# Optimization experiments

Hardware: AMD Instinct MI355X
Metric: run time of the kernel (lower is better)

Reference implementation:

```python
import jax, jax.numpy as jnp
import numpy as np
import math

N_HEADS = 4
N_ITERS = 2  # SSFormer n=2; each loop iteration recomputes the same values (no feedback in the original code)
BN_EPS = 1e-5


def _attention(q, k, v):
    """SSTransformer: multi-head cross-attention over flattened spatial dims.
    q,k,v: [B, C, H, W] -> returns [B, C, L] with L = H*W.
    """
    b, c = q.shape[0], q.shape[1]
    L = q.shape[2] * q.shape[3]
    ch = c // N_HEADS
    scale = 1.0 / math.sqrt(math.sqrt(ch))
    qf = (q.reshape(b * N_HEADS, ch, L) * scale)
    kf = (k.reshape(b * N_HEADS, ch, L) * scale)
    vf = v.reshape(b * N_HEADS, ch, L)
    # weight: [B*H, t, s]
    w = jnp.einsum('bct,bcs->bts', qf, kf)
    w = jax.nn.softmax(w.astype(jnp.float32), axis=-1).astype(w.dtype)
    a = jnp.einsum('bts,bcs->bct', w, vf)
    return a.reshape(b, c, L)


def setup_inputs() -> dict:
    key = jax.random.key(0)
    k1, k2, k3, k4 = jax.random.split(key, 4)
    B, C, H, W = 8, 512, 32, 32
    c = jax.random.normal(k1, (B, C, H, W), dtype=jnp.float32)
    e = jax.random.normal(k2, (B, C, H, W), dtype=jnp.float32)
    conv_w = jax.random.normal(k3, (C, C, 1, 1), dtype=jnp.float32) / math.sqrt(C)
    conv_b = jax.random.normal(k4, (C,), dtype=jnp.float32) * 0.02
    bn_gamma = jnp.ones((C,), dtype=jnp.float32)
    bn_beta = jnp.zeros((C,), dtype=jnp.float32)
    return {"c": c, "e": e, "conv_w": conv_w, "conv_b": conv_b,
            "bn_gamma": bn_gamma, "bn_beta": bn_beta}


def reference(c, e, conv_w, conv_b, bn_gamma, bn_beta):
    bs, ch, h, w = c.shape
    L = h * w
    for _ in range(N_ITERS):
        _c = _attention(e, c, c)                       # [B, C, L]
        _e = _attention(_c.reshape(bs, ch, h, w), e, e)  # [B, C, L]
    _e = _e.reshape(bs, ch, h, w)
    # Proj: 1x1 conv + BatchNorm2d (training-mode batch stats) + Swish
    x = jnp.einsum('oc,bchw->bohw', conv_w.reshape(ch, ch), _e) + conv_b[None, :, None, None]
    mean = jnp.mean(x, axis=(0, 2, 3), keepdims=True)
    var = jnp.var(x, axis=(0, 2, 3), keepdims=True)
    xn = (x - mean) * jax.lax.rsqrt(var + BN_EPS)
    xn = xn * bn_gamma[None, :, None, None] + bn_beta[None, :, None, None]
    return xn * jax.nn.sigmoid(xn)
```

## Files before the change

### kernel.cpp

```cpp
#include <hip/hip_runtime.h>
#include <hip/hip_bf16.h>

typedef __attribute__((ext_vector_type(8))) short short8;
typedef __attribute__((ext_vector_type(4))) float floatx4;
typedef __attribute__((ext_vector_type(4))) float f32x4;
typedef unsigned short u16;
typedef unsigned int u32;
typedef __attribute__((ext_vector_type(2))) unsigned int u32x2;
typedef __attribute__((ext_vector_type(4))) unsigned int u32x4;
typedef __attribute__((ext_vector_type(8))) unsigned short ushort8;

#define LSEQ 1024
#define CHD  128
#define CEXP 0.12751744900425577f
#define THR_RAW 62.73318f

static __device__ __forceinline__ u16 f2b(float f) {
  __hip_bfloat16 h = __float2bfloat16(f);
  return *reinterpret_cast<u16*>(&h);
}
static __device__ __forceinline__ u32 cvtpk(float a, float b) {
  u32 r;
  asm("v_cvt_pk_bf16_f32 %0, %1, %2" : "=v"(r) : "v"(a), "v"(b));
  return r;
}
static __device__ __forceinline__ float exp2f_fast(float x) {
  float r;
  asm("v_exp_f32 %0, %1" : "=v"(r) : "v"(x));
  return r;
}
static __device__ __forceinline__ void gl_lds16(const void* g, void* l) {
  __builtin_amdgcn_global_load_lds((__attribute__((address_space(1))) const void*)g,
                                   (__attribute__((address_space(3))) void*)l, 16, 0, 0);
}

__global__ __launch_bounds__(256) void k_prep(const float* __restrict__ cin,
                                              const float* __restrict__ ein,
                                              u16* __restrict__ cV, u16* __restrict__ cT,
                                              u16* __restrict__ eV, u16* __restrict__ eT) {
  __shared__ u16 tile[32][72];
  int z = blockIdx.z;
  const float* in = (z < 32) ? cin : ein;
  u16* outV = (z < 32) ? cV : eV;
  u16* outT = (z < 32) ? cT : eT;
  int bh = z & 31, c0 = blockIdx.y * 32, s0 = blockIdx.x * 64;
  int tid = threadIdx.x;
  int cl = tid >> 3, sc = tid & 7;
  size_t off = ((size_t)bh * CHD + c0 + cl) * LSEQ + s0 + sc * 8;
  f32x4 a = *(const f32x4*)(in + off);
  f32x4 b = *(const f32x4*)(in + off + 4);
  u32x4 u;
  u[0] = cvtpk(a[0], a[1]); u[1] = cvtpk(a[2], a[3]);
  u[2] = cvtpk(b[0], b[1]); u[3] = cvtpk(b[2], b[3]);
  *(u32x4*)(outV + off) = u;
  *(u32x4*)&tile[cl][sc * 8] = u;
  __syncthreads();
  int sl = tid >> 2, cc = tid & 3;
  ushort8 v;
#pragma unroll
  for (int j = 0; j < 8; ++j) v[j] = tile[cc * 8 + j][sl];
  *(ushort8*)(outT + ((size_t)bh * LSEQ + s0 + sl) * CHD + c0 + cc * 8) = v;
}

__global__ __launch_bounds__(256) void k_wcvt(const float* __restrict__ w, u16* __restrict__ wb,
                                              float* __restrict__ zbuf ) {
  int tid = threadIdx.x;
  int base = (blockIdx.x * 256 + tid) * 8;
  f32x4 a = *(const f32x4*)(w + base);
  f32x4 b = *(const f32x4*)(w + base + 4);
  u32x4 u;
  u[0] = cvtpk(a[0], a[1]); u[1] = cvtpk(a[2], a[3]);
  u[2] = cvtpk(b[0], b[1]); u[3] = cvtpk(b[2], b[3]);
  *(u32x4*)(wb + base) = u;
  if (blockIdx.x == 0) {
    f32x4 z; z[0]=0.f; z[1]=0.f; z[2]=0.f; z[3]=0.f;
    *(f32x4*)(zbuf + tid * 4) = z;
  }
}

__global__ __launch_bounds__(256) void k_attn(const u16* __restrict__ eT,
                                              const u16* __restrict__ cT,
                                              const u16* __restrict__ cV,
                                              const u16* __restrict__ eV,
                                              u16* __restrict__ outT) {
  __shared__ char ldsbuf[73728];

  int bh = blockIdx.x, tt = blockIdx.y;
  int tid = threadIdx.x;
  int w = tid >> 6, lane = tid & 63;
  int lo = lane & 15, hi = lane >> 4;
  int t0 = tt * 64 + w * 16;

  char* pw = ldsbuf + 65536 + w * 2048 + lo * 128;
  int sw = (lo & 7) << 4;

  auto stageK = [&](int buf, int sb, const char* kTb) {
    char* dst = ldsbuf + buf * 16384;
#pragma unroll
    for (int it = 0; it < 4; ++it) {
      int bb = it * 4096 + tid * 16;
      int row = bb >> 8;
      int cb = (bb & 255) ^ ((row & 7) << 4);
      gl_lds16(kTb + (size_t)(sb * 64 + row) * 256 + cb, dst + bb);
    }
  };
  auto stageV = [&](int buf, int sb, const char* vb) {
    char* dst = ldsbuf + 32768 + buf * 16384;
#pragma unroll
    for (int it = 0; it < 4; ++it) {
      int bb = it * 4096 + tid * 16;
      int row = bb >> 7;
      int cb = (bb & 127) ^ ((row & 7) << 4);
      gl_lds16(vb + (size_t)row * 2048 + sb * 128 + cb, dst + bb);
    }
  };

  short8 bq[4];
  floatx4 oacc[8];
  float m_r, l_r;

  auto flash = [&](const char* kTb, const char* vb) {
    m_r = -1e30f; l_r = 0.f;
#pragma unroll
    for (int i = 0; i < 8; ++i) { oacc[i][0]=0.f; oacc[i][1]=0.f; oacc[i][2]=0.f; oacc[i][3]=0.f; }
    stageK(0, 0, kTb); stageV(0, 0, vb);
    __syncthreads();
    int cur = 0;
    for (int sb = 0; sb < 16; ++sb) {
      if (sb < 15) { stageK(cur ^ 1, sb + 1, kTb); stageV(cur ^ 1, sb + 1, vb); }
      const char* ldsK = ldsbuf + cur * 16384;
      const char* ldsV = ldsbuf + 32768 + cur * 16384;

      float sa[4][4];
      __builtin_amdgcn_s_setprio(1);
#pragma unroll
      for (int ss = 0; ss < 4; ++ss) {
        floatx4 acc; acc[0]=0.f; acc[1]=0.f; acc[2]=0.f; acc[3]=0.f;
        int row = ss * 16 + lo;
#pragma unroll
        for (int ks = 0; ks < 4; ++ks) {
          int cbyte = (ks * 64 + hi * 16) ^ ((row & 7) << 4);
          short8 a = *(const short8*)(ldsK + row * 256 + cbyte);
          acc = __builtin_amdgcn_mfma_f32_16x16x32_bf16(a, bq[ks], acc, 0, 0, 0);
        }
#pragma unroll
        for (int r = 0; r < 4; ++r) sa[ss][r] = acc[r];
      }
      __builtin_amdgcn_s_setprio(0);

      float x0 = fmaxf(fmaxf(sa[0][0], sa[0][1]), sa[0][2]);
      float x1 = fmaxf(fmaxf(sa[0][3], sa[1][0]), sa[1][1]);
      float x2 = fmaxf(fmaxf(sa[1][2], sa[1][3]), sa[2][0]);
      float x3 = fmaxf(fmaxf(sa[2][1], sa[2][2]), sa[2][3]);
      float x4 = fmaxf(fmaxf(sa[3][0], sa[3][1]), sa[3][2]);
      float bm = fmaxf(fmaxf(fmaxf(x0, x1), fmaxf(x2, x3)), fmaxf(x4, sa[3][3]));
      bm = fmaxf(bm, __shfl_xor(bm, 16));
      bm = fmaxf(bm, __shfl_xor(bm, 32));

      bool stay = __all(bm - m_r <= THR_RAW);
      if (!stay) {
        float mn = fmaxf(m_r, bm);
        float corr = exp2f_fast((m_r - mn) * CEXP);
        m_r = mn;
        l_r *= corr;
#pragma unroll
        for (int i = 0; i < 8; ++i) {
          oacc[i][0] *= corr; oacc[i][1] *= corr; oacc[i][2] *= corr; oacc[i][3] *= corr;
        }
      }
      float mnC = m_r * CEXP;

      float rs = 0.f;
#pragma unroll
      for (int ss = 0; ss < 4; ++ss)
#pragma unroll
        for (int r = 0; r < 4; ++r) {
          float p = exp2f_fast(__builtin_fmaf(sa[ss][r], CEXP, -mnC));
          sa[ss][r] = p;
          rs += p;
        }
      rs += __shfl_xor(rs, 16);
      rs += __shfl_xor(rs, 32);
      l_r += rs;

#pragma unroll
      for (int ss = 0; ss < 4; ++ss) {
        u32x2 pk;
        pk[0] = cvtpk(sa[ss][0], sa[ss][1]);
        pk[1] = cvtpk(sa[ss][2], sa[ss][3]);
        *(u32x2*)(pw + ((ss * 32 + hi * 8) ^ sw)) = pk;
      }
      asm volatile("" ::: "memory");

      short8 bp0 = *(const short8*)(pw + ((hi * 16) ^ sw));
      short8 bp1 = *(const short8*)(pw + ((64 + hi * 16) ^ sw));
      __builtin_amdgcn_s_setprio(1);
#pragma unroll
      for (int mt = 0; mt < 8; ++mt) {
        int crow = mt * 16 + lo;
        const char* va = ldsV + crow * 128;
        int vsw = (crow & 7) << 4;
        short8 a0 = *(const short8*)(va + ((hi * 16) ^ vsw));
        short8 a1 = *(const short8*)(va + ((64 + hi * 16) ^ vsw));
        oacc[mt] = __builtin_amdgcn_mfma_f32_16x16x32_bf16(a0, bp0, oacc[mt], 0, 0, 0);
        oacc[mt] = __builtin_amdgcn_mfma_f32_16x16x32_bf16(a1, bp1, oacc[mt], 0, 0, 0);
      }
      __builtin_amdgcn_s_setprio(0);
      __syncthreads();
      cur ^= 1;
    }
  };

  const u16* qbase = eT + ((size_t)bh * LSEQ + t0 + lo) * CHD + hi * 8;
#pragma unroll
  for (int ks = 0; ks < 4; ++ks) bq[ks] = *(const short8*)(qbase + ks * 32);

  flash((const char*)(cT + (size_t)bh * LSEQ * CHD),
        (const char*)(cV + (size_t)bh * CHD * LSEQ));

  {
    float inv = 1.0f / l_r;
    char* ot = ldsbuf + w * 4096;
#pragma unroll
    for (int mt = 0; mt < 8; ++mt) {
      u32x2 pk;
      pk[0] = cvtpk(oacc[mt][0] * inv, oacc[mt][1] * inv);
      pk[1] = cvtpk(oacc[mt][2] * inv, oacc[mt][3] * inv);
      *(u32x2*)(ot + lo * 256 + ((mt * 32 + hi * 8) ^ ((lo & 7) << 4))) = pk;
    }
    asm volatile("" ::: "memory");
#pragma unroll
    for (int ks = 0; ks < 4; ++ks) {
      int cb = (ks * 64 + hi * 16) ^ ((lo & 7) << 4);
      bq[ks] = *(const short8*)(ot + lo * 256 + cb);
    }
  }
  __syncthreads();

  flash((const char*)(eT + (size_t)bh * LSEQ * CHD),
        (const char*)(eV + (size_t)bh * CHD * LSEQ));

  float inv = 1.0f / l_r;
  char* ot = ldsbuf + w * 4096;
#pragma unroll
  for (int mt = 0; mt < 8; ++mt) {
    u32x2 pk;
    pk[0] = cvtpk(oacc[mt][0] * inv, oacc[mt][1] * inv);
    pk[1] = cvtpk(oacc[mt][2] * inv, oacc[mt][3] * inv);
    *(u32x2*)(ot + lo * 256 + ((mt * 32 + hi * 8) ^ ((lo & 7) << 4))) = pk;
  }
  asm volatile("" ::: "memory");
  u16* orow = outT + ((size_t)bh * LSEQ + t0 + lo) * CHD;
#pragma unroll
  for (int it = 0; it < 4; ++it) {
    int cb = (it * 64 + hi * 16) ^ ((lo & 7) << 4);
    ushort8 d = *(const ushort8*)(ot + lo * 256 + cb);
    *(ushort8*)(orow + it * 32 + hi * 8) = d;
  }
}

__global__ __launch_bounds__(256) void k_proj(const u16* __restrict__ Wm,
                                              const u16* __restrict__ eT,
                                              const float* __restrict__ bias,
                                              u16* __restrict__ x,
                                              float* __restrict__ chsum,
                                              float* __restrict__ chsq) {
  __shared__ char lds[65536];
  int lt = blockIdx.x, ot = blockIdx.y;
  int b = lt >> 3;
  int l0b = (lt & 7) * 128;
  int o0 = ot * 128;
  int tid = threadIdx.x, w = tid >> 6, lane = tid & 63, lo = lane & 15, hi = lane >> 4;
  int wm = w >> 1, wn = w & 1;
  const char* Wb = (const char*)Wm;
  const char* eTb = (const char*)eT;

  auto stageA = [&](int buf, int kb) {
    char* dst = lds + buf * 16384;
#pragma unroll
    for (int it = 0; it < 4; ++it) {
      int bb = it * 4096 + tid * 16;
      int row = bb >> 7;
      int cb = (bb & 127) ^ ((row & 7) << 4);
      gl_lds16(Wb + (size_t)(o0 + row) * 1024 + kb * 128 + cb, dst + bb);
    }
  };
  auto stageB = [&](int buf, int kb) {
    char* dst = lds + 32768 + buf * 16384;
    int page = b * 4 + (kb >> 1);
    int choff = (kb & 1) * 128;
#pragma unroll
    for (int it = 0; it < 4; ++it) {
      int bb = it * 4096 + tid * 16;
      int row = bb >> 7;
      int cb = (bb & 127) ^ ((row & 7) << 4);
      gl_lds16(eTb + ((size_t)page * 1024 + l0b + row) * 256 + choff + cb, dst + bb);
    }
  };

  floatx4 acc[4][4];
#pragma unroll
  for (int i = 0; i < 4; ++i)
#pragma unroll
    for (int j = 0; j < 4; ++j) { acc[i][j][0]=0.f; acc[i][j][1]=0.f; acc[i][j][2]=0.f; acc[i][j][3]=0.f; }

  stageA(0, 0); stageB(0, 0);
  __syncthreads();
  int cur = 0;

  for (int kb = 0; kb < 8; ++kb) {
    if (kb < 7) { stageA(cur ^ 1, kb + 1); stageB(cur ^ 1, kb + 1); }
    const char* A = lds + cur * 16384;
    const char* B = lds + 32768 + cur * 16384;
#pragma unroll
    for (int kk = 0; kk < 2; ++kk) {
      short8 af[4], bf[4];
#pragma unroll
      for (int mi = 0; mi < 4; ++mi) {
        int row = wm * 64 + mi * 16 + lo;
        af[mi] = *(const short8*)(A + row * 128 + ((kk * 64 + hi * 16) ^ ((row & 7) << 4)));
      }
#pragma unroll
      for (int ni = 0; ni < 4; ++ni) {
        int row = wn * 64 + ni * 16 + lo;
        bf[ni] = *(const short8*)(B + row * 128 + ((kk * 64 + hi * 16) ^ ((row & 7) << 4)));
      }
      __builtin_amdgcn_s_setprio(1);
#pragma unroll
      for (int mi = 0; mi < 4; ++mi)
#pragma unroll
        for (int ni = 0; ni < 4; ++ni)
          acc[mi][ni] = __builtin_amdgcn_mfma_f32_16x16x32_bf16(af[mi], bf[ni], acc[mi][ni], 0, 0, 0);
      __builtin_amdgcn_s_setprio(0);
    }
    __syncthreads();
    cur ^= 1;
  }

#pragma unroll
  for (int mi = 0; mi < 4; ++mi) {
#pragma unroll
    for (int r = 0; r < 4; ++r) {
      int o = o0 + wm * 64 + mi * 16 + hi * 4 + r;
      float bv = bias[o];
      float s = 0.f, q = 0.f;
#pragma unroll
      for (int ni = 0; ni < 4; ++ni) {
        float xv = acc[mi][ni][r] + bv;
        x[((size_t)b * 512 + o) * LSEQ + l0b + wn * 64 + ni * 16 + lo] = f2b(xv);
        s += xv; q += xv * xv;
      }
#pragma unroll
      for (int d = 1; d < 16; d <<= 1) { s += __shfl_xor(s, d); q += __shfl_xor(q, d); }
      if (lo == 0) {
        atomicAdd(&chsum[o], s);
        atomicAdd(&chsq[o], q);
      }
    }
  }
}

__global__ __launch_bounds__(256) void k_final(const u16* __restrict__ x,
                                               const float* __restrict__ chsum,
                                               const float* __restrict__ chsq,
                                               const float* __restrict__ gamma,
                                               const float* __restrict__ beta,
                                               float* __restrict__ out) {
  int idx = blockIdx.x * 256 + threadIdx.x;
  int base = idx * 8;
  int ch = (base >> 10) & 511;
  const float invn = 1.0f / 8192.0f;
  float mean = chsum[ch] * invn;
  float var = chsq[ch] * invn - mean * mean;
  float rstd = rsqrtf(var + 1e-5f);
  float sc = gamma[ch] * rstd;
  float sh = beta[ch] - mean * sc;
  ushort8 vx = *(const ushort8*)(x + base);
  f32x4 o0, o1;
#pragma unroll
  for (int j = 0; j < 8; ++j) {
    union { u32 i; float f; } cv; cv.i = ((u32)vx[j]) << 16;
    float xn = cv.f * sc + sh;
    float sg = 1.0f / (1.0f + __expf(-xn));
    float r = xn * sg;
    if (j < 4) o0[j] = r; else o1[j - 4] = r;
  }
  *(f32x4*)(out + base) = o0;
  *(f32x4*)(out + base + 4) = o1;
}

extern "C" void kernel_launch(void* const* d_in, const int* in_sizes, int n_in,
                              void* d_out, int out_size, void* d_ws, size_t ws_size,
                              hipStream_t stream) {
  const float* c     = (const float*)d_in[0];
  const float* e     = (const float*)d_in[1];
  const float* Wf    = (const float*)d_in[2];
  const float* bias  = (const float*)d_in[3];
  const float* gamma = (const float*)d_in[4];
  const float* beta  = (const float*)d_in[5];
  float* outp = (float*)d_out;

  char* ws = (char*)d_ws;
  const size_t TB = (size_t)32 * 1024 * 128 * 2;
  u16* eT  = (u16*)(ws);
  u16* cT  = (u16*)(ws + TB);
  u16* cV  = (u16*)(ws + 2 * TB);
  u16* eV  = (u16*)(ws + 3 * TB);
  u16* xT  = (u16*)(ws + 4 * TB);
  u16* Wbf = (u16*)(ws + 5 * TB);
  float* chsum = (float*)(ws + 5 * TB + (1 << 20));
  float* chsq  = chsum + 512;
  u16* x   = (u16*)(ws + 6 * TB);

  dim3 tb(256);

  k_wcvt<<<dim3(128), tb, 0, stream>>>(Wf, Wbf, chsum);
  k_prep<<<dim3(16, 4, 64), tb, 0, stream>>>(c, e, cV, cT, eV, eT);
  k_attn<<<dim3(32, 16), tb, 0, stream>>>(eT, cT, cV, eV, xT);
  k_proj<<<dim3(64, 4), tb, 0, stream>>>(Wbf, xT, bias, x, chsum, chsq);
  k_final<<<dim3(2048), tb, 0, stream>>>(x, chsum, chsq, gamma, beta, outp);
}
```

Baseline: 111.6 us.

## Fold weight conversion into prep kernel and use split-waitcnt barriers in pipelines

The separate weight-conversion launch is merged into the prep kernel as two extra z-slices, removing one kernel launch. In the attention and projection double-buffered loops, the trailing __syncthreads is replaced by a raw barrier, then the next stage's loads are issued, then a partial vmcnt wait and a second barrier. The current buffer's loads are waited on with vmcnt(8) while the prefetch stays in flight. The intent is to stop waiting on all outstanding memory at each barrier. It relies on an exact count of outstanding loads and adds a second barrier per iteration.

```diff
diff --git a/kernel.cpp b/kernel.cpp
--- a/kernel.cpp
+++ b/kernel.cpp
@@ -36,15 +36,32 @@
 
 __global__ __launch_bounds__(256) void k_prep(const float* __restrict__ cin,
                                               const float* __restrict__ ein,
+                                              const float* __restrict__ Wf,
                                               u16* __restrict__ cV, u16* __restrict__ cT,
-                                              u16* __restrict__ eV, u16* __restrict__ eT) {
+                                              u16* __restrict__ eV, u16* __restrict__ eT,
+                                              u16* __restrict__ wb, float* __restrict__ zbuf) {
   __shared__ u16 tile[32][72];
   int z = blockIdx.z;
+  int tid = threadIdx.x;
+  if (z >= 64) {
+    int wblk = (z - 64) * 64 + blockIdx.y * 16 + blockIdx.x;
+    int base = (wblk * 256 + tid) * 8;
+    f32x4 a = *(const f32x4*)(Wf + base);
+    f32x4 b = *(const f32x4*)(Wf + base + 4);
+    u32x4 u;
+    u[0] = cvtpk(a[0], a[1]); u[1] = cvtpk(a[2], a[3]);
+    u[2] = cvtpk(b[0], b[1]); u[3] = cvtpk(b[2], b[3]);
+    *(u32x4*)(wb + base) = u;
+    if (wblk == 0) {
+      f32x4 zz; zz[0]=0.f; zz[1]=0.f; zz[2]=0.f; zz[3]=0.f;
+      *(f32x4*)(zbuf + tid * 4) = zz;
+    }
+    return;
+  }
   const float* in = (z < 32) ? cin : ein;
   u16* outV = (z < 32) ? cV : eV;
   u16* outT = (z < 32) ? cT : eT;
   int bh = z & 31, c0 = blockIdx.y * 32, s0 = blockIdx.x * 64;
-  int tid = threadIdx.x;
   int cl = tid >> 3, sc = tid & 7;
   size_t off = ((size_t)bh * CHD + c0 + cl) * LSEQ + s0 + sc * 8;
   f32x4 a = *(const f32x4*)(in + off);
@@ -62,22 +79,6 @@
   *(ushort8*)(outT + ((size_t)bh * LSEQ + s0 + sl) * CHD + c0 + cc * 8) = v;
 }
 
-__global__ __launch_bounds__(256) void k_wcvt(const float* __restrict__ w, u16* __restrict__ wb,
-                                              float* __restrict__ zbuf ) {
-  int tid = threadIdx.x;
-  int base = (blockIdx.x * 256 + tid) * 8;
-  f32x4 a = *(const f32x4*)(w + base);
-  f32x4 b = *(const f32x4*)(w + base + 4);
-  u32x4 u;
-  u[0] = cvtpk(a[0], a[1]); u[1] = cvtpk(a[2], a[3]);
-  u[2] = cvtpk(b[0], b[1]); u[3] = cvtpk(b[2], b[3]);
-  *(u32x4*)(wb + base) = u;
-  if (blockIdx.x == 0) {
-    f32x4 z; z[0]=0.f; z[1]=0.f; z[2]=0.f; z[3]=0.f;
-    *(f32x4*)(zbuf + tid * 4) = z;
-  }
-}
-
 __global__ __launch_bounds__(256) void k_attn(const u16* __restrict__ eT,
                                               const u16* __restrict__ cT,
                                               const u16* __restrict__ cV,
@@ -124,10 +125,14 @@
 #pragma unroll
     for (int i = 0; i < 8; ++i) { oacc[i][0]=0.f; oacc[i][1]=0.f; oacc[i][2]=0.f; oacc[i][3]=0.f; }
     stageK(0, 0, kTb); stageV(0, 0, vb);
-    __syncthreads();
-    int cur = 0;
     for (int sb = 0; sb < 16; ++sb) {
+      int cur = sb & 1;
+      __builtin_amdgcn_s_barrier();
       if (sb < 15) { stageK(cur ^ 1, sb + 1, kTb); stageV(cur ^ 1, sb + 1, vb); }
+      if (sb < 15) { asm volatile("s_waitcnt vmcnt(8)" ::: "memory"); }
+      else         { asm volatile("s_waitcnt vmcnt(0)" ::: "memory"); }
+      __builtin_amdgcn_s_barrier();
+
       const char* ldsK = ldsbuf + cur * 16384;
       const char* ldsV = ldsbuf + 32768 + cur * 16384;
 
@@ -206,8 +211,6 @@
         oacc[mt] = __builtin_amdgcn_mfma_f32_16x16x32_bf16(a1, bp1, oacc[mt], 0, 0, 0);
       }
       __builtin_amdgcn_s_setprio(0);
-      __syncthreads();
-      cur ^= 1;
     }
   };
 
@@ -305,11 +308,14 @@
     for (int j = 0; j < 4; ++j) { acc[i][j][0]=0.f; acc[i][j][1]=0.f; acc[i][j][2]=0.f; acc[i][j][3]=0.f; }
 
   stageA(0, 0); stageB(0, 0);
-  __syncthreads();
-  int cur = 0;
 
   for (int kb = 0; kb < 8; ++kb) {
+    int cur = kb & 1;
+    __builtin_amdgcn_s_barrier();
     if (kb < 7) { stageA(cur ^ 1, kb + 1); stageB(cur ^ 1, kb + 1); }
+    if (kb < 7) { asm volatile("s_waitcnt vmcnt(8)" ::: "memory"); }
+    else        { asm volatile("s_waitcnt vmcnt(0)" ::: "memory"); }
+    __builtin_amdgcn_s_barrier();
     const char* A = lds + cur * 16384;
     const char* B = lds + 32768 + cur * 16384;
 #pragma unroll
@@ -333,8 +339,6 @@
           acc[mi][ni] = __builtin_amdgcn_mfma_f32_16x16x32_bf16(af[mi], bf[ni], acc[mi][ni], 0, 0, 0);
       __builtin_amdgcn_s_setprio(0);
     }
-    __syncthreads();
-    cur ^= 1;
   }
 
 #pragma unroll
@@ -414,8 +418,7 @@
 
   dim3 tb(256);
 
-  k_wcvt<<<dim3(128), tb, 0, stream>>>(Wf, Wbf, chsum);
-  k_prep<<<dim3(16, 4, 64), tb, 0, stream>>>(c, e, cV, cT, eV, eT);
+  k_prep<<<dim3(16, 4, 66), tb, 0, stream>>>(c, e, Wf, cV, cT, eV, eT, Wbf, chsum);
   k_attn<<<dim3(32, 16), tb, 0, stream>>>(eT, cT, cV, eV, xT);
   k_proj<<<dim3(64, 4), tb, 0, stream>>>(Wbf, xT, bias, x, chsum, chsq);
   k_final<<<dim3(2048), tb, 0, stream>>>(x, chsum, chsq, gamma, beta, outp);
```

Measured after the change: 109.2 us. 1.02x faster.
